# Kernel tuning notes

Measured on AMD Instinct MI355X. Metric: run time of the kernel, lower is better.

## Reference

```python
import jax, jax.numpy as jnp
import numpy as np

C_IN = 256
RED = 8
C_QK = C_IN // RED  # 32


def setup_inputs() -> dict:
    key = jax.random.key(0)
    ks = jax.random.split(key, 8)
    B, C, H, W = 4, C_IN, 64, 64
    x = jax.random.normal(ks[0], (B, C, H, W), dtype=jnp.float32)
    # 1x1 conv weights stored as (out_ch, in_ch); biases (out_ch,)
    s = 1.0 / np.sqrt(C)
    wq = jax.random.uniform(ks[1], (C_QK, C), minval=-s, maxval=s, dtype=jnp.float32)
    bq = jax.random.uniform(ks[2], (C_QK,), minval=-s, maxval=s, dtype=jnp.float32)
    wk = jax.random.uniform(ks[3], (C_QK, C), minval=-s, maxval=s, dtype=jnp.float32)
    bk = jax.random.uniform(ks[4], (C_QK,), minval=-s, maxval=s, dtype=jnp.float32)
    wv = jax.random.uniform(ks[5], (C, C), minval=-s, maxval=s, dtype=jnp.float32)
    bv = jax.random.uniform(ks[6], (C,), minval=-s, maxval=s, dtype=jnp.float32)
    # nn.Parameter(torch.zeros(1)) -> use small nonzero so gradients flow in tests
    gamma = jnp.full((1,), 0.5, dtype=jnp.float32)
    return {"x": x, "wq": wq, "bq": bq, "wk": wk, "bk": bk,
            "wv": wv, "bv": bv, "gamma": gamma}


def reference(x, wq, bq, wk, bk, wv, bv, gamma):
    B, C, H, W = x.shape
    N = H * W
    xf = x.reshape(B, C, N)                                  # (B,C,N)
    # 1x1 convs == per-pixel linear projections over channels
    q = jnp.einsum('dc,bcn->bdn', wq, xf) + bq[None, :, None]  # (B,Cqk,N)
    k = jnp.einsum('dc,bcn->bdn', wk, xf) + bk[None, :, None]  # (B,Cqk,N)
    v = jnp.einsum('oc,bcn->bon', wv, xf) + bv[None, :, None]  # (B,C,N)
    # attention[b,i,j] = <q[:,i], k[:,j]> ; softmax over j (no scaling, as in source)
    scores = jnp.einsum('bdi,bdj->bij', q, k)                 # (B,N,N)
    attn = jax.nn.softmax(scores, axis=-1)
    # out[b,c,i] = sum_j v[b,c,j] * attn[b,i,j]
    out = jnp.einsum('bcj,bij->bci', v, attn).reshape(B, C, H, W)
    return gamma * out + x
```

## Files before the change

kernel.cpp:

```cpp
#include <hip/hip_runtime.h>
#include <hip/hip_bf16.h>


#define NB     4
#define CC     256
#define CQK    32
#define NPIX   4096
#define NCHUNK 4
#define CHUNK  (NPIX / NCHUNK)
#define NT     (CHUNK / 64)

typedef float floatx4 __attribute__((ext_vector_type(4)));
typedef short shortx4 __attribute__((ext_vector_type(4)));
typedef short shortx8 __attribute__((ext_vector_type(8)));

__device__ __forceinline__ short f2bf(float f) {
  unsigned u = __float_as_uint(f);
  u += 0x7fffu + ((u >> 16) & 1u);
  return (short)(u >> 16);
}
__device__ __forceinline__ float bf2f(unsigned short u) {
  return __uint_as_float((unsigned)u << 16);
}
__device__ __forceinline__ unsigned pk2bf(float a, float b) {
  union { __hip_bfloat162 h; unsigned u; } cv;
  cv.h = __float22bfloat162_rn(make_float2(a, b));
  return cv.u;
}
__device__ __forceinline__ void gload16(const void* g, void* l) {
  __builtin_amdgcn_global_load_lds(
      (const __attribute__((address_space(1))) void*)g,
      (__attribute__((address_space(3))) void*)l, 16, 0, 0);
}

__global__ __launch_bounds__(256) void projx_kernel(
    const float* __restrict__ x,
    const float* __restrict__ wq, const float* __restrict__ bq,
    const float* __restrict__ wk, const float* __restrict__ bk,
    const float* __restrict__ wv, const float* __restrict__ bv,
    short* __restrict__ Qb, short* __restrict__ Kb, short* __restrict__ Vb)
{
  __shared__ short U[256 * 72 + 64 * 72];

  const int gid = blockIdx.x;
  const int b = gid >> 6, n0 = (gid & 63) * 64;
  const int t = threadIdx.x, lane = t & 63, w = t >> 6;
  const int lo = lane & 15, hi = lane >> 4;

  {
    const int cl = t >> 2;
    const int nq = (t & 3) * 16;
#pragma unroll
    for (int rr = 0; rr < 4; rr++) {
      const float* src = x + ((size_t)(b * CC + rr * 64 + cl)) * NPIX + n0 + nq;
      floatx4 v[4];
#pragma unroll
      for (int q = 0; q < 4; q++) v[q] = *(const floatx4*)(src + q * 4);
#pragma unroll
      for (int i = 0; i < 16; i++) {
        const int n = nq + i;
        U[n * 256 + rr * 64 + (cl ^ ((i & 7) << 3))] = f2bf(v[i >> 2][i & 3]);
      }
    }
  }
  __syncthreads();

  const float* wrow[5];
#pragma unroll
  for (int rt = 0; rt < 5; rt++) {
    const int o = w * 80 + rt * 16 + lo;
    wrow[rt] = (o < 32) ? (wq + (size_t)o * CC)
             : (o < 64) ? (wk + (size_t)(o - 32) * CC)
                        : (wv + (size_t)(o - 64) * CC);
  }

  floatx4 acc[5][4];
#pragma unroll
  for (int r = 0; r < 5; r++)
#pragma unroll
    for (int c = 0; c < 4; c++) acc[r][c] = (floatx4){0.f, 0.f, 0.f, 0.f};

#pragma unroll
  for (int c0 = 0; c0 < CC; c0 += 32) {
    shortx8 bf[4];
#pragma unroll
    for (int ct = 0; ct < 4; ct++) {
      const int n = ct * 16 + lo;
      const int c = c0 + hi * 8;
      bf[ct] = *(const shortx8*)
          &U[n * 256 + (c & 192) + ((c & 63) ^ ((n & 7) << 3))];
    }
#pragma unroll
    for (int rt = 0; rt < 5; rt++) {
      const float* ap = wrow[rt] + c0 + hi * 8;
      floatx4 a0 = *(const floatx4*)ap;
      floatx4 a1 = *(const floatx4*)(ap + 4);
      if (w == 0 && rt < 2) {
        a0 *= 1.44269504088896f; a1 *= 1.44269504088896f;
      }
      union { shortx8 s; unsigned u[4]; } au;
      au.u[0] = pk2bf(a0[0], a0[1]);
      au.u[1] = pk2bf(a0[2], a0[3]);
      au.u[2] = pk2bf(a1[0], a1[1]);
      au.u[3] = pk2bf(a1[2], a1[3]);
#pragma unroll
      for (int ct = 0; ct < 4; ct++)
        acc[rt][ct] = __builtin_amdgcn_mfma_f32_16x16x32_bf16(au.s, bf[ct], acc[rt][ct], 0, 0, 0);
    }
  }

  __syncthreads();

#pragma unroll
  for (int rt = 0; rt < 5; rt++) {
#pragma unroll
    for (int j = 0; j < 4; j++) {
      const int o = w * 80 + rt * 16 + hi * 4 + j;
      const float bs = (o < 32) ? bq[o] * 1.44269504088896f
                     : (o < 64) ? bk[o - 32] : bv[o - 64];
#pragma unroll
      for (int ct = 0; ct < 4; ct++) {
        const int n = ct * 16 + lo;
        const short hv = f2bf(acc[rt][ct][j] + bs);
        if (o < 64) U[256 * 72 + n * 72 + o] = hv;
        else        U[(o - 64) * 72 + n] = hv;
      }
    }
  }
  __syncthreads();

#pragma unroll
  for (int it = 0; it < 8; it++) {
    const int ov = it * 32 + (t >> 3);
    const int seg = (t & 7) * 8;
    const shortx8 d = *(const shortx8*)&U[ov * 72 + seg];
    *(shortx8*)(Vb + ((size_t)(b * CC + ov)) * NPIX + n0 + seg) = d;
  }
  if (w < 2) {
    const int n = lane;
    short* dst = (w == 0 ? Qb : Kb) + ((size_t)(b * NPIX + n0 + n)) * CQK;
    const int off = 256 * 72 + n * 72 + w * 32;
#pragma unroll
    for (int s = 0; s < 4; s++) {
      const shortx8 d = *(const shortx8*)&U[off + s * 8];
      *(shortx8*)(dst + s * 8) = d;
    }
  }
}

__global__ __launch_bounds__(256, 2) void attn_kernel(
    const short* __restrict__ Qb, const short* __restrict__ Kb,
    const short* __restrict__ Vb,
    short* __restrict__ Opart, float* __restrict__ Lpart)
{
  __shared__ short Vl[2][16384];
  __shared__ short Kl[2][2048];
  __shared__ short Pl[4][1024];

  const int bc = blockIdx.x & 15, qt = blockIdx.x >> 4;
  const int b = bc & 3, ch = bc >> 2;
  const int q0 = qt * 128, kv0 = ch * CHUNK;
  const int tid = threadIdx.x, lane = tid & 63, w = tid >> 6;
  const int lo = lane & 15, hi = lane >> 4;

  const short* Kc = Kb + ((size_t)(b * NPIX + kv0)) * CQK;
  const short* Vc = Vb + (size_t)b * CC * NPIX + kv0;

  shortx8 qf[2];
#pragma unroll
  for (int qs = 0; qs < 2; qs++)
    qf[qs] = *(const shortx8*)(
        Qb + ((size_t)(b * NPIX + q0 + w * 32 + qs * 16 + lo)) * CQK + hi * 8);

  const int cV = w * 64 + (lane >> 3);
  const int pcV = lane & 7;
  const int kvK = w * 16 + (lane >> 2);
  const int lcK = (lane & 3) ^ ((kvK >> 1) & 3);

  floatx4 oacc[2][16];
#pragma unroll
  for (int qs = 0; qs < 2; qs++)
#pragma unroll
    for (int i = 0; i < 16; i++) oacc[qs][i] = (floatx4){0.f, 0.f, 0.f, 0.f};
  float l[2] = {0.f, 0.f};
  const floatx4 zero4 = (floatx4){0.f, 0.f, 0.f, 0.f};

#pragma unroll
  for (int i = 0; i < 8; i++) {
    const int c = cV + i * 8;
    gload16(Vc + (size_t)c * NPIX + (pcV ^ (c & 7)) * 8, &Vl[0][w * 4096 + i * 512]);
  }
  gload16(Kc + (size_t)kvK * CQK + lcK * 8, &Kl[0][w * 512]);
  __syncthreads();

  for (int t = 0; t < NT; t++) {
    const int buf = t & 1;

    if (t + 1 < NT) {
      const int j0n = (t + 1) * 64;
#pragma unroll
      for (int i = 0; i < 8; i++) {
        const int c = cV + i * 8;
        gload16(Vc + (size_t)c * NPIX + j0n + (pcV ^ (c & 7)) * 8,
                &Vl[buf ^ 1][w * 4096 + i * 512]);
      }
      gload16(Kc + (size_t)(j0n + kvK) * CQK + lcK * 8, &Kl[buf ^ 1][w * 512]);
    }

    floatx4 s[2][4];
#pragma unroll
    for (int ct = 0; ct < 4; ct++) {
      const int kv = ct * 16 + lo;
      const shortx8 kf = *(const shortx8*)
          &Kl[buf][kv * 32 + ((hi * 8) ^ (((kv >> 1) & 3) << 3))];
      s[0][ct] = __builtin_amdgcn_mfma_f32_16x16x32_bf16(kf, qf[0], zero4, 0, 0, 0);
      s[1][ct] = __builtin_amdgcn_mfma_f32_16x16x32_bf16(kf, qf[1], zero4, 0, 0, 0);
    }

    shortx8 pb[2][2];
#pragma unroll
    for (int qs = 0; qs < 2; qs++) {
      float rs = 0.f;
#pragma unroll
      for (int ct = 0; ct < 4; ct++) {
        const float p0 = exp2f(s[qs][ct][0]), p1 = exp2f(s[qs][ct][1]);
        const float p2 = exp2f(s[qs][ct][2]), p3 = exp2f(s[qs][ct][3]);
        rs += (p0 + p1) + (p2 + p3);
        uint2 u;
        u.x = pk2bf(p0, p1);
        u.y = pk2bf(p2, p3);
        *(uint2*)&Pl[w][lo * 64 + ((ct * 16 + hi * 4) ^ ((lo & 7) << 3))] = u;
      }
#pragma unroll
      for (int h = 0; h < 2; h++)
        pb[qs][h] = *(const shortx8*)
            &Pl[w][lo * 64 + ((h * 32 + hi * 8) ^ ((lo & 7) << 3))];
      rs += __shfl_xor(rs, 16);
      rs += __shfl_xor(rs, 32);
      l[qs] += rs;
    }

#pragma unroll
    for (int ctv = 0; ctv < 16; ctv++) {
      const int c = ctv * 16 + lo;
      const int swz = (c & 7) << 3;
      const shortx8 va0 = *(const shortx8*)&Vl[buf][c * 64 + ((hi * 8) ^ swz)];
      const shortx8 va1 = *(const shortx8*)&Vl[buf][c * 64 + ((32 + hi * 8) ^ swz)];
      oacc[0][ctv] = __builtin_amdgcn_mfma_f32_16x16x32_bf16(va0, pb[0][0], oacc[0][ctv], 0, 0, 0);
      oacc[0][ctv] = __builtin_amdgcn_mfma_f32_16x16x32_bf16(va1, pb[0][1], oacc[0][ctv], 0, 0, 0);
      oacc[1][ctv] = __builtin_amdgcn_mfma_f32_16x16x32_bf16(va0, pb[1][0], oacc[1][ctv], 0, 0, 0);
      oacc[1][ctv] = __builtin_amdgcn_mfma_f32_16x16x32_bf16(va1, pb[1][1], oacc[1][ctv], 0, 0, 0);
    }

    __syncthreads();
  }

  if (hi == 0) {
    Lpart[(size_t)bc * NPIX + q0 + w * 32 + lo] = l[0];
    Lpart[(size_t)bc * NPIX + q0 + w * 32 + 16 + lo] = l[1];
  }
#pragma unroll
  for (int qs = 0; qs < 2; qs++) {
    const int n = q0 + w * 32 + qs * 16 + lo;
#pragma unroll
    for (int ctv = 0; ctv < 16; ctv++)
#pragma unroll
      for (int j = 0; j < 4; j++) {
        const int c = ctv * 16 + hi * 4 + j;
        Opart[((size_t)bc * CC + c) * NPIX + n] = f2bf(oacc[qs][ctv][j]);
      }
  }
}

__global__ __launch_bounds__(256) void combine_kernel(
    const short* __restrict__ Opart, const float* __restrict__ Lpart,
    const float* __restrict__ x, const float* __restrict__ gamma,
    float* __restrict__ out)
{
  __shared__ float linv[512];
  const int gid = blockIdx.x;
  const int b = gid >> 7;
  const int c0 = ((gid >> 3) & 15) * 16;
  const int n0 = (gid & 7) * 512;
  const int t = threadIdx.x;

  if (t < 128) {
    const int n = n0 + t * 4;
    floatx4 sum = (floatx4){0.f, 0.f, 0.f, 0.f};
#pragma unroll
    for (int k = 0; k < NCHUNK; k++)
      sum += *(const floatx4*)(Lpart + (size_t)(k * NB + b) * NPIX + n);
#pragma unroll
    for (int i = 0; i < 4; i++) linv[t * 4 + i] = 1.0f / sum[i];
  }
  __syncthreads();

  const float g = gamma[0];
  const int il = t & 63, cw = t >> 6;
  const int n = n0 + il * 8;
  float li[8];
#pragma unroll
  for (int j = 0; j < 8; j++) li[j] = linv[il * 8 + j];

#pragma unroll
  for (int i = 0; i < 4; i++) {
    const int c = c0 + cw * 4 + i;
    float acc[8];
#pragma unroll
    for (int j = 0; j < 8; j++) acc[j] = 0.f;
#pragma unroll
    for (int k = 0; k < NCHUNK; k++) {
      const shortx8 o = *(const shortx8*)(
          Opart + ((size_t)((k * NB + b) * CC + c)) * NPIX + n);
#pragma unroll
      for (int j = 0; j < 8; j++) acc[j] += bf2f((unsigned short)o[j]);
    }
    const size_t idx = ((size_t)(b * CC + c)) * NPIX + n;
    const floatx4 x0 = *(const floatx4*)(x + idx);
    const floatx4 x1 = *(const floatx4*)(x + idx + 4);
    floatx4 r0, r1;
#pragma unroll
    for (int j = 0; j < 4; j++) {
      r0[j] = g * (acc[j] * li[j]) + x0[j];
      r1[j] = g * (acc[j + 4] * li[j + 4]) + x1[j];
    }
    *(floatx4*)(out + idx) = r0;
    *(floatx4*)(out + idx + 4) = r1;
  }
}

extern "C" void kernel_launch(void* const* d_in, const int* in_sizes, int n_in,
                              void* d_out, int out_size, void* d_ws, size_t ws_size,
                              hipStream_t stream) {
  const float* x     = (const float*)d_in[0];
  const float* wq    = (const float*)d_in[1];
  const float* bq    = (const float*)d_in[2];
  const float* wk    = (const float*)d_in[3];
  const float* bk    = (const float*)d_in[4];
  const float* wv    = (const float*)d_in[5];
  const float* bv    = (const float*)d_in[6];
  const float* gamma = (const float*)d_in[7];
  float* out = (float*)d_out;

  char* p = (char*)d_ws;
  short* Qb    = (short*)p; p += (size_t)NB * NPIX * CQK * 2;
  short* Kb    = (short*)p; p += (size_t)NB * NPIX * CQK * 2;
  short* Vb    = (short*)p; p += (size_t)NB * CC * NPIX * 2;
  short* Opart = (short*)p; p += (size_t)(NCHUNK * NB) * CC * NPIX * 2;
  float* Lpart = (float*)p; p += (size_t)(NCHUNK * NB) * NPIX * 4;

  projx_kernel<<<dim3(256), dim3(256), 0, stream>>>(x, wq, bq, wk, bk, wv, bv, Qb, Kb, Vb);
  attn_kernel<<<dim3(512), dim3(256), 0, stream>>>(Qb, Kb, Vb, Opart, Lpart);
  combine_kernel<<<dim3(512), dim3(256), 0, stream>>>(Opart, Lpart, x, gamma, out);
}
```

Measured before the change: 161.2 us.

## Shrink projection and combine tiles for more blocks; raise MFMA priority in attention

The projection kernel now processes 16 pixels per block instead of 64 and launches 1024 blocks. It writes V straight to global memory from the accumulators, with no shared-memory transpose. The combine kernel halves its tile to launch 1024 blocks, and the attention PV MFMA loop is wrapped in s_setprio to favour the matrix issue. The aim is better occupancy and load balance in the small kernels, at the cost of more weight reloads per pixel and uncoalesced 2-byte V stores.

Result: slower. 182.3 us (+13.1%).

```diff
diff --git a/kernel.cpp b/kernel.cpp
--- a/kernel.cpp
+++ b/kernel.cpp
@@ -40,26 +40,26 @@
     const float* __restrict__ wv, const float* __restrict__ bv,
     short* __restrict__ Qb, short* __restrict__ Kb, short* __restrict__ Vb)
 {
-  __shared__ short U[256 * 72 + 64 * 72];
+  __shared__ short T[16 * 256];
+  __shared__ short SQK[16 * 72];
 
   const int gid = blockIdx.x;
-  const int b = gid >> 6, n0 = (gid & 63) * 64;
+  const int b = gid >> 8, n0 = (gid & 255) * 16;
   const int t = threadIdx.x, lane = t & 63, w = t >> 6;
   const int lo = lane & 15, hi = lane >> 4;
 
   {
+    const int nq = (t & 3) * 4;
     const int cl = t >> 2;
-    const int nq = (t & 3) * 16;
 #pragma unroll
     for (int rr = 0; rr < 4; rr++) {
-      const float* src = x + ((size_t)(b * CC + rr * 64 + cl)) * NPIX + n0 + nq;
-      floatx4 v[4];
-#pragma unroll
-      for (int q = 0; q < 4; q++) v[q] = *(const floatx4*)(src + q * 4);
-#pragma unroll
-      for (int i = 0; i < 16; i++) {
+      const int c = rr * 64 + cl;
+      const floatx4 v = *(const floatx4*)(
+          x + ((size_t)(b * CC + c)) * NPIX + n0 + nq);
+#pragma unroll
+      for (int i = 0; i < 4; i++) {
         const int n = nq + i;
-        U[n * 256 + rr * 64 + (cl ^ ((i & 7) << 3))] = f2bf(v[i >> 2][i & 3]);
+        T[n * 256 + rr * 64 + (cl ^ ((n & 7) << 3))] = f2bf(v[i]);
       }
     }
   }
@@ -74,22 +74,15 @@
                         : (wv + (size_t)(o - 64) * CC);
   }
 
-  floatx4 acc[5][4];
-#pragma unroll
-  for (int r = 0; r < 5; r++)
-#pragma unroll
-    for (int c = 0; c < 4; c++) acc[r][c] = (floatx4){0.f, 0.f, 0.f, 0.f};
+  floatx4 acc[5];
+#pragma unroll
+  for (int r = 0; r < 5; r++) acc[r] = (floatx4){0.f, 0.f, 0.f, 0.f};
 
 #pragma unroll
   for (int c0 = 0; c0 < CC; c0 += 32) {
-    shortx8 bf[4];
-#pragma unroll
-    for (int ct = 0; ct < 4; ct++) {
-      const int n = ct * 16 + lo;
-      const int c = c0 + hi * 8;
-      bf[ct] = *(const shortx8*)
-          &U[n * 256 + (c & 192) + ((c & 63) ^ ((n & 7) << 3))];
-    }
+    const int c = c0 + hi * 8;
+    const shortx8 bf = *(const shortx8*)
+        &T[lo * 256 + (c & 192) + ((c & 63) ^ ((lo & 7) << 3))];
 #pragma unroll
     for (int rt = 0; rt < 5; rt++) {
       const float* ap = wrow[rt] + c0 + hi * 8;
@@ -103,12 +96,9 @@
       au.u[1] = pk2bf(a0[2], a0[3]);
       au.u[2] = pk2bf(a1[0], a1[1]);
       au.u[3] = pk2bf(a1[2], a1[3]);
-#pragma unroll
-      for (int ct = 0; ct < 4; ct++)
-        acc[rt][ct] = __builtin_amdgcn_mfma_f32_16x16x32_bf16(au.s, bf[ct], acc[rt][ct], 0, 0, 0);
-    }
-  }
-
+      acc[rt] = __builtin_amdgcn_mfma_f32_16x16x32_bf16(au.s, bf, acc[rt], 0, 0, 0);
+    }
+  }
   __syncthreads();
 
 #pragma unroll
@@ -118,33 +108,20 @@
       const int o = w * 80 + rt * 16 + hi * 4 + j;
       const float bs = (o < 32) ? bq[o] * 1.44269504088896f
                      : (o < 64) ? bk[o - 32] : bv[o - 64];
-#pragma unroll
-      for (int ct = 0; ct < 4; ct++) {
-        const int n = ct * 16 + lo;
-        const short hv = f2bf(acc[rt][ct][j] + bs);
-        if (o < 64) U[256 * 72 + n * 72 + o] = hv;
-        else        U[(o - 64) * 72 + n] = hv;
-      }
-    }
-  }
-  __syncthreads();
-
-#pragma unroll
-  for (int it = 0; it < 8; it++) {
-    const int ov = it * 32 + (t >> 3);
-    const int seg = (t & 7) * 8;
-    const shortx8 d = *(const shortx8*)&U[ov * 72 + seg];
-    *(shortx8*)(Vb + ((size_t)(b * CC + ov)) * NPIX + n0 + seg) = d;
-  }
-  if (w < 2) {
-    const int n = lane;
-    short* dst = (w == 0 ? Qb : Kb) + ((size_t)(b * NPIX + n0 + n)) * CQK;
-    const int off = 256 * 72 + n * 72 + w * 32;
-#pragma unroll
-    for (int s = 0; s < 4; s++) {
-      const shortx8 d = *(const shortx8*)&U[off + s * 8];
-      *(shortx8*)(dst + s * 8) = d;
-    }
+      const short hv = f2bf(acc[rt][j] + bs);
+      if (o < 64) SQK[lo * 72 + o] = hv;
+      else        Vb[((size_t)(b * CC + (o - 64))) * NPIX + n0 + lo] = hv;
+    }
+  }
+  __syncthreads();
+
+  if (t < 128) {
+    const int isK = t >> 6;
+    const int flat = (t & 63) * 8;
+    const int n = flat >> 5, o = flat & 31;
+    const shortx8 d = *(const shortx8*)&SQK[n * 72 + isK * 32 + o];
+    short* base = isK ? Kb : Qb;
+    *(shortx8*)(base + ((size_t)(b * NPIX + n0 + n)) * CQK + o) = d;
   }
 }
 
@@ -240,6 +217,7 @@
       l[qs] += rs;
     }
 
+    __builtin_amdgcn_s_setprio(1);
 #pragma unroll
     for (int ctv = 0; ctv < 16; ctv++) {
       const int c = ctv * 16 + lo;
@@ -251,6 +229,7 @@
       oacc[1][ctv] = __builtin_amdgcn_mfma_f32_16x16x32_bf16(va0, pb[1][0], oacc[1][ctv], 0, 0, 0);
       oacc[1][ctv] = __builtin_amdgcn_mfma_f32_16x16x32_bf16(va1, pb[1][1], oacc[1][ctv], 0, 0, 0);
     }
+    __builtin_amdgcn_s_setprio(0);
 
     __syncthreads();
   }
@@ -277,14 +256,14 @@
     const float* __restrict__ x, const float* __restrict__ gamma,
     float* __restrict__ out)
 {
-  __shared__ float linv[512];
+  __shared__ float linv[256];
   const int gid = blockIdx.x;
-  const int b = gid >> 7;
-  const int c0 = ((gid >> 3) & 15) * 16;
-  const int n0 = (gid & 7) * 512;
+  const int b = gid >> 8;
+  const int c0 = ((gid >> 4) & 15) * 16;
+  const int n0 = (gid & 15) * 256;
   const int t = threadIdx.x;
 
-  if (t < 128) {
+  if (t < 64) {
     const int n = n0 + t * 4;
     floatx4 sum = (floatx4){0.f, 0.f, 0.f, 0.f};
 #pragma unroll
@@ -296,15 +275,15 @@
   __syncthreads();
 
   const float g = gamma[0];
-  const int il = t & 63, cw = t >> 6;
+  const int il = t & 31, cw = t >> 5;
   const int n = n0 + il * 8;
   float li[8];
 #pragma unroll
   for (int j = 0; j < 8; j++) li[j] = linv[il * 8 + j];
 
 #pragma unroll
-  for (int i = 0; i < 4; i++) {
-    const int c = c0 + cw * 4 + i;
+  for (int i = 0; i < 2; i++) {
+    const int c = c0 + cw * 2 + i;
     float acc[8];
 #pragma unroll
     for (int j = 0; j < 8; j++) acc[j] = 0.f;
@@ -349,7 +328,7 @@
   short* Opart = (short*)p; p += (size_t)(NCHUNK * NB) * CC * NPIX * 2;
   float* Lpart = (float*)p; p += (size_t)(NCHUNK * NB) * NPIX * 4;
 
-  projx_kernel<<<dim3(256), dim3(256), 0, stream>>>(x, wq, bq, wk, bk, wv, bv, Qb, Kb, Vb);
+  projx_kernel<<<dim3(1024), dim3(256), 0, stream>>>(x, wq, bq, wk, bk, wv, bv, Qb, Kb, Vb);
   attn_kernel<<<dim3(512), dim3(256), 0, stream>>>(Qb, Kb, Vb, Opart, Lpart);
-  combine_kernel<<<dim3(512), dim3(256), 0, stream>>>(Opart, Lpart, x, gamma, out);
-}
+  combine_kernel<<<dim3(1024), dim3(256), 0, stream>>>(Opart, Lpart, x, gamma, out);
+}
```
